# Kernel optimization log

Hardware: AMD Instinct MI355X
Metric: run time of the kernel (lower is better)

## Reference

```python
import jax, jax.numpy as jnp
import numpy as np

Q, V = 16384, 4096  # query batch (captions), video batch


def setup_inputs() -> dict:
    key = jax.random.key(0)
    q2ctx_scores = jax.random.normal(key, (Q, V), dtype=jnp.float32)
    # each query labeled with a video; arange % V guarantees every video has >=1 query
    labels = jnp.arange(Q, dtype=jnp.int64) % V
    return {"q2ctx_scores": q2ctx_scores, "labels": labels}


def reference(q2ctx_scores, labels):
    # q2ctx_scores: [Q, V], labels: [Q] int in [0, V)
    Qn, Vn = q2ctx_scores.shape
    # t2v: nominator is the matched score (logsumexp over a single element is identity)
    s = jnp.take_along_axis(q2ctx_scores, labels[:, None], axis=1)[:, 0]  # [Q]
    t2v_denominator = jax.nn.logsumexp(q2ctx_scores, axis=1)              # [Q]
    # v2t nominator: segmented logsumexp of matched scores grouped by video label
    m = jax.ops.segment_max(s, labels, num_segments=Vn)                   # [V]
    seg_sum = jax.ops.segment_sum(jnp.exp(s - m[labels]), labels, num_segments=Vn)
    v2t_nominator = m + jnp.log(seg_sum)                                  # [V]
    v2t_denominator = jax.nn.logsumexp(q2ctx_scores, axis=0)              # [V]
    return jnp.mean(t2v_denominator - s) + jnp.mean(v2t_denominator - v2t_nominator)
```

## Files before the change

kernel.cpp:

```cpp
#include <hip/hip_runtime.h>
#include <hip/hip_bf16.h>


#define QN 16384
#define VN 4096

#define COLPART_OFF 0
#define T2V_OFF     (512 * VN)
#define NOMSUM_OFF  (T2V_OFF + QN)
#define COLSUM_OFF  (NOMSUM_OFF + VN)
#define ACC_OFF     (COLSUM_OFF + VN)

__global__ __launch_bounds__(512) void init_pass(float* __restrict__ ws) {
    int i = blockIdx.x * 512 + threadIdx.x;
    int n = VN + VN + 8;
    if (i < n) ws[NOMSUM_OFF + i] = 0.0f;
}

__global__ __launch_bounds__(512, 4) void main_pass(const float* __restrict__ scores,
                                                    const int* __restrict__ labels,
                                                    float* __restrict__ ws) {
    float* colPartial = ws + COLPART_OFF;
    float* t2v        = ws + T2V_OFF;
    float* nomsum     = ws + NOMSUM_OFF;

    __shared__ __align__(16) float lcolT[VN];
    const int tid  = threadIdx.x;
    const int wid  = tid >> 6;
    const int lane = tid & 63;

    for (int i = tid; i < VN; i += 512) lcolT[i] = 0.0f;
    __syncthreads();

    const int gw   = blockIdx.x * 8 + wid;
    const int row0 = gw * 4;
    const float4* p0 = reinterpret_cast<const float4*>(scores + (size_t)row0 * VN);
    const float4* p1 = p0 + 1024;
    const float4* p2 = p0 + 2048;
    const float4* p3 = p0 + 3072;

    float ra0 = 0.f, ra1 = 0.f, ra2 = 0.f, ra3 = 0.f;

#pragma unroll 4
    for (int c = 0; c < 16; ++c) {
        const int idx = c * 64 + lane;
        float4 x0 = p0[idx];
        float4 x1 = p1[idx];
        float4 x2 = p2[idx];
        float4 x3 = p3[idx];
        float4 e0, e1, e2, e3;
        e0.x = __expf(x0.x); e0.y = __expf(x0.y); e0.z = __expf(x0.z); e0.w = __expf(x0.w);
        e1.x = __expf(x1.x); e1.y = __expf(x1.y); e1.z = __expf(x1.z); e1.w = __expf(x1.w);
        e2.x = __expf(x2.x); e2.y = __expf(x2.y); e2.z = __expf(x2.z); e2.w = __expf(x2.w);
        e3.x = __expf(x3.x); e3.y = __expf(x3.y); e3.z = __expf(x3.z); e3.w = __expf(x3.w);
        ra0 += (e0.x + e0.y) + (e0.z + e0.w);
        ra1 += (e1.x + e1.y) + (e1.z + e1.w);
        ra2 += (e2.x + e2.y) + (e2.z + e2.w);
        ra3 += (e3.x + e3.y) + (e3.z + e3.w);
        atomicAdd(&lcolT[0 * 1024 + idx], (e0.x + e1.x) + (e2.x + e3.x));
        atomicAdd(&lcolT[1 * 1024 + idx], (e0.y + e1.y) + (e2.y + e3.y));
        atomicAdd(&lcolT[2 * 1024 + idx], (e0.z + e1.z) + (e2.z + e3.z));
        atomicAdd(&lcolT[3 * 1024 + idx], (e0.w + e1.w) + (e2.w + e3.w));
    }

#pragma unroll
    for (int off = 32; off >= 1; off >>= 1) {
        ra0 += __shfl_down(ra0, off);
        ra1 += __shfl_down(ra1, off);
        ra2 += __shfl_down(ra2, off);
        ra3 += __shfl_down(ra3, off);
    }

    float s_val = 0.f;
    if (lane < 4) {
        const int lab = labels[row0 + lane];
        s_val = scores[(size_t)(row0 + lane) * VN + lab];
        unsafeAtomicAdd(&nomsum[lab], __expf(s_val));
    }
    const float s0 = __shfl(s_val, 0);
    const float s1 = __shfl(s_val, 1);
    const float s2 = __shfl(s_val, 2);
    const float s3 = __shfl(s_val, 3);
    if (lane == 0) {
        t2v[row0 + 0] = __logf(ra0) - s0;
        t2v[row0 + 1] = __logf(ra1) - s1;
        t2v[row0 + 2] = __logf(ra2) - s2;
        t2v[row0 + 3] = __logf(ra3) - s3;
    }

    __syncthreads();
    float4* dst = reinterpret_cast<float4*>(colPartial + (size_t)blockIdx.x * VN);
    const float4* src = reinterpret_cast<const float4*>(lcolT);
    dst[tid]       = src[tid];
    dst[tid + 512] = src[tid + 512];
}

__global__ __launch_bounds__(256) void reduce_pass(float* __restrict__ ws) {
    const float* colPartial = ws + COLPART_OFF;
    const float* t2v        = ws + T2V_OFF;
    float* colsum = ws + COLSUM_OFF;
    float* acc    = ws + ACC_OFF;
    const int tid = threadIdx.x;

    if (blockIdx.x < 256) {
        const int cg  = blockIdx.x & 15;
        const int bg  = blockIdx.x >> 4;
        const int col = cg * 256 + tid;
        float sum = 0.0f;
#pragma unroll 4
        for (int b = bg * 32; b < bg * 32 + 32; ++b)
            sum += colPartial[(size_t)b * VN + col];
        unsafeAtomicAdd(&colsum[col], sum);
    } else {
        const int idx = (blockIdx.x - 256) * 256 + tid;
        float v = t2v[idx];
#pragma unroll
        for (int off = 32; off >= 1; off >>= 1)
            v += __shfl_down(v, off);
        __shared__ float red[4];
        const int wid = tid >> 6, lane = tid & 63;
        if (lane == 0) red[wid] = v;
        __syncthreads();
        if (tid == 0)
            unsafeAtomicAdd(&acc[0], (red[0] + red[1]) + (red[2] + red[3]));
    }
}

__global__ __launch_bounds__(256) void final_pass(const float* __restrict__ ws,
                                                  float* __restrict__ out) {
    const float* nomsum = ws + NOMSUM_OFF;
    const float* colsum = ws + COLSUM_OFF;
    const float* acc    = ws + ACC_OFF;
    const int tid = threadIdx.x;

    float local = 0.0f;
    for (int c = tid; c < VN; c += 256)
        local += __logf(colsum[c]) - __logf(nomsum[c]);
#pragma unroll
    for (int off = 32; off >= 1; off >>= 1)
        local += __shfl_down(local, off);
    __shared__ float red[4];
    const int wid = tid >> 6, lane = tid & 63;
    if (lane == 0) red[wid] = local;
    __syncthreads();
    if (tid == 0) {
        const float v2t = (red[0] + red[1]) + (red[2] + red[3]);
        out[0] = acc[0] * (1.0f / QN) + v2t * (1.0f / VN);
    }
}

extern "C" void kernel_launch(void* const* d_in, const int* in_sizes, int n_in,
                              void* d_out, int out_size, void* d_ws, size_t ws_size,
                              hipStream_t stream) {
    const float* scores = (const float*)d_in[0];
    const int*   labels = (const int*)d_in[1];
    float* ws  = (float*)d_ws;
    float* out = (float*)d_out;

    init_pass<<<(2 * VN + 8 + 511) / 512, 512, 0, stream>>>(ws);
    main_pass<<<512, 512, 0, stream>>>(scores, labels, ws);
    reduce_pass<<<320, 256, 0, stream>>>(ws);
    final_pass<<<1, 256, 0, stream>>>(ws, out);
}
```

Baseline: 373.9 us.

## Halve main_pass block size and software-prefetch next row chunk

The main pass now launches 1024 blocks of 256 threads instead of 512 blocks of 512, so each block covers 16 rows. This doubles the per-block column partials written to workspace and read back by the reduce pass. The column loop is fully unrolled and double-buffers its loads, issuing the next chunk's float4 reads before computing exp and doing the LDS atomics on the current chunk, to hide memory latency. The trade-off is higher register pressure and more partial-sum traffic in exchange for more resident blocks and overlap.

New measurement: 376.6 us. About the same (+0.7%).

```diff
diff --git a/kernel.cpp b/kernel.cpp
--- a/kernel.cpp
+++ b/kernel.cpp
@@ -4,9 +4,10 @@
 
 #define QN 16384
 #define VN 4096
+#define NBLK 1024
 
 #define COLPART_OFF 0
-#define T2V_OFF     (512 * VN)
+#define T2V_OFF     (NBLK * VN)
 #define NOMSUM_OFF  (T2V_OFF + QN)
 #define COLSUM_OFF  (NOMSUM_OFF + VN)
 #define ACC_OFF     (COLSUM_OFF + VN)
@@ -17,7 +18,7 @@
     if (i < n) ws[NOMSUM_OFF + i] = 0.0f;
 }
 
-__global__ __launch_bounds__(512, 4) void main_pass(const float* __restrict__ scores,
+__global__ __launch_bounds__(256, 4) void main_pass(const float* __restrict__ scores,
                                                     const int* __restrict__ labels,
                                                     float* __restrict__ ws) {
     float* colPartial = ws + COLPART_OFF;
@@ -29,10 +30,10 @@
     const int wid  = tid >> 6;
     const int lane = tid & 63;
 
-    for (int i = tid; i < VN; i += 512) lcolT[i] = 0.0f;
+    for (int i = tid; i < VN; i += 256) lcolT[i] = 0.0f;
     __syncthreads();
 
-    const int gw   = blockIdx.x * 8 + wid;
+    const int gw   = blockIdx.x * 4 + wid;
     const int row0 = gw * 4;
     const float4* p0 = reinterpret_cast<const float4*>(scores + (size_t)row0 * VN);
     const float4* p1 = p0 + 1024;
@@ -41,18 +42,30 @@
 
     float ra0 = 0.f, ra1 = 0.f, ra2 = 0.f, ra3 = 0.f;
 
-#pragma unroll 4
+    float4 xa0 = p0[lane];
+    float4 xa1 = p1[lane];
+    float4 xa2 = p2[lane];
+    float4 xa3 = p3[lane];
+
+#pragma unroll
     for (int c = 0; c < 16; ++c) {
+        float4 xb0, xb1, xb2, xb3;
+        if (c < 15) {
+            const int nidx = (c + 1) * 64 + lane;
+            xb0 = p0[nidx];
+            xb1 = p1[nidx];
+            xb2 = p2[nidx];
+            xb3 = p3[nidx];
+        } else {
+            xb0 = xa0; xb1 = xa1; xb2 = xa2; xb3 = xa3;
+        }
+
         const int idx = c * 64 + lane;
-        float4 x0 = p0[idx];
-        float4 x1 = p1[idx];
-        float4 x2 = p2[idx];
-        float4 x3 = p3[idx];
         float4 e0, e1, e2, e3;
-        e0.x = __expf(x0.x); e0.y = __expf(x0.y); e0.z = __expf(x0.z); e0.w = __expf(x0.w);
-        e1.x = __expf(x1.x); e1.y = __expf(x1.y); e1.z = __expf(x1.z); e1.w = __expf(x1.w);
-        e2.x = __expf(x2.x); e2.y = __expf(x2.y); e2.z = __expf(x2.z); e2.w = __expf(x2.w);
-        e3.x = __expf(x3.x); e3.y = __expf(x3.y); e3.z = __expf(x3.z); e3.w = __expf(x3.w);
+        e0.x = __expf(xa0.x); e0.y = __expf(xa0.y); e0.z = __expf(xa0.z); e0.w = __expf(xa0.w);
+        e1.x = __expf(xa1.x); e1.y = __expf(xa1.y); e1.z = __expf(xa1.z); e1.w = __expf(xa1.w);
+        e2.x = __expf(xa2.x); e2.y = __expf(xa2.y); e2.z = __expf(xa2.z); e2.w = __expf(xa2.w);
+        e3.x = __expf(xa3.x); e3.y = __expf(xa3.y); e3.z = __expf(xa3.z); e3.w = __expf(xa3.w);
         ra0 += (e0.x + e0.y) + (e0.z + e0.w);
         ra1 += (e1.x + e1.y) + (e1.z + e1.w);
         ra2 += (e2.x + e2.y) + (e2.z + e2.w);
@@ -61,6 +74,8 @@
         atomicAdd(&lcolT[1 * 1024 + idx], (e0.y + e1.y) + (e2.y + e3.y));
         atomicAdd(&lcolT[2 * 1024 + idx], (e0.z + e1.z) + (e2.z + e3.z));
         atomicAdd(&lcolT[3 * 1024 + idx], (e0.w + e1.w) + (e2.w + e3.w));
+
+        xa0 = xb0; xa1 = xb1; xa2 = xb2; xa3 = xb3;
     }
 
 #pragma unroll
@@ -92,7 +107,9 @@
     float4* dst = reinterpret_cast<float4*>(colPartial + (size_t)blockIdx.x * VN);
     const float4* src = reinterpret_cast<const float4*>(lcolT);
     dst[tid]       = src[tid];
+    dst[tid + 256] = src[tid + 256];
     dst[tid + 512] = src[tid + 512];
+    dst[tid + 768] = src[tid + 768];
 }
 
 __global__ __launch_bounds__(256) void reduce_pass(float* __restrict__ ws) {
@@ -106,9 +123,10 @@
         const int cg  = blockIdx.x & 15;
         const int bg  = blockIdx.x >> 4;
         const int col = cg * 256 + tid;
+        const int per = NBLK / 16;
         float sum = 0.0f;
 #pragma unroll 4
-        for (int b = bg * 32; b < bg * 32 + 32; ++b)
+        for (int b = bg * per; b < bg * per + per; ++b)
             sum += colPartial[(size_t)b * VN + col];
         unsafeAtomicAdd(&colsum[col], sum);
     } else {
@@ -158,7 +176,7 @@
     float* out = (float*)d_out;
 
     init_pass<<<(2 * VN + 8 + 511) / 512, 512, 0, stream>>>(ws);
-    main_pass<<<512, 512, 0, stream>>>(scores, labels, ws);
+    main_pass<<<NBLK, 256, 0, stream>>>(scores, labels, ws);
     reduce_pass<<<320, 256, 0, stream>>>(ws);
     final_pass<<<1, 256, 0, stream>>>(ws, out);
 }
```
